# Optimization experiments

Hardware: AMD Instinct MI355X
Metric: run time of the kernel (lower is better)

## Reference

```python
import jax, jax.numpy as jnp
import numpy as np

E = 8          # num_experts
K = 2          # top_k
CAP = 0.8      # capacity_ratio
LN_EPS = 1e-6


def setup_inputs() -> dict:
    key = jax.random.key(0)
    ks = jax.random.split(key, 6)
    N, C, H, W = 64, 384, 32, 32
    Hd = 4 * C
    x = jax.random.normal(ks[0], (N, C, H, W), jnp.float32)
    conv_w = jax.random.normal(ks[1], (7, 7, 1, C), jnp.float32) * 0.05  # HWIO, depthwise
    conv_b = jnp.zeros((C,), jnp.float32)
    ln_g = jnp.ones((C,), jnp.float32)
    ln_b = jnp.zeros((C,), jnp.float32)
    gate_w = jax.random.normal(ks[2], (E, C), jnp.float32) * 0.02
    w1 = jax.random.normal(ks[3], (E, C, Hd), jnp.float32) * 0.02
    b1 = jnp.zeros((E, Hd), jnp.float32)
    w2 = jax.random.normal(ks[4], (E, Hd, C), jnp.float32) * 0.02
    b2 = jnp.zeros((E, C), jnp.float32)
    layer_scale = jnp.ones((C, 1, 1), jnp.float32) * 1e-6
    return dict(x=x, conv_w=conv_w, conv_b=conv_b, ln_g=ln_g, ln_b=ln_b,
                gate_w=gate_w, w1=w1, b1=b1, w2=w2, b2=b2, layer_scale=layer_scale)


def reference(x, conv_w, conv_b, ln_g, ln_b, gate_w, w1, b1, w2, b2, layer_scale):
    N, C, H, W = x.shape
    # depthwise 7x7 conv, pad 3
    h = jax.lax.conv_general_dilated(
        x, conv_w, window_strides=(1, 1), padding=[(3, 3), (3, 3)],
        dimension_numbers=('NCHW', 'HWIO', 'NCHW'), feature_group_count=C)
    h = h + conv_b[None, :, None, None]
    h = h.transpose(0, 2, 3, 1)  # NHWC
    # LayerNorm over channels
    mu = h.mean(-1, keepdims=True)
    var = ((h - mu) ** 2).mean(-1, keepdims=True)
    h = (h - mu) * jax.lax.rsqrt(var + LN_EPS) * ln_g + ln_b

    T = N * H * W
    x_flat = h.reshape(T, C)

    # Router (eval mode: no aux loss)
    logits = x_flat @ gate_w.T                    # [T, E]
    probs = jax.nn.softmax(logits, axis=-1)
    priority = probs.max(-1)                       # [T]
    topv, topi = jax.lax.top_k(logits, K)          # [T, K]
    weights = jax.nn.softmax(topv, axis=-1)        # [T, K]
    order = jnp.argsort(-priority)                 # descending priority

    # Dispatch: layout k-major like torch (order.repeat(K), topi[order].T.reshape(-1))
    token_idx = jnp.tile(order, K)                 # [M]
    expert_id = topi[order].T.reshape(-1)          # [M]
    gate = weights[order].T.reshape(-1)            # [M]
    M = K * T
    perm = jnp.argsort(expert_id, stable=True)
    token_idx = token_idx[perm]
    expert_id = expert_id[perm]
    gate = gate[perm]

    Be = int(round(K * T * CAP / E))               # static capacity per expert
    counts = jnp.bincount(expert_id, length=E)
    starts = jnp.cumsum(counts) - counts
    pos = jnp.arange(M) - starts[expert_id]
    keep = pos < Be
    slot = jnp.where(keep, expert_id * Be + pos, E * Be)  # dropped -> trash slot

    disp_tok = jnp.zeros((E * Be + 1,), jnp.int32).at[slot].set(token_idx.astype(jnp.int32))
    disp_gate = jnp.zeros((E * Be + 1,), x_flat.dtype).at[slot].set(gate)
    disp_tok = disp_tok[:-1].reshape(E, Be)
    disp_gate = disp_gate[:-1].reshape(E, Be)      # 0 for unfilled slots

    # Grouped expert MLP
    x_e = x_flat[disp_tok]                         # [E, Be, C]
    hid = jax.nn.gelu(jnp.einsum('ebc,ech->ebh', x_e, w1) + b1[:, None, :], approximate=False)
    y = (jnp.einsum('ebh,ehc->ebc', hid, w2) + b2[:, None, :]) * disp_gate[:, :, None]

    # Combine (scatter-add); unfilled slots contribute 0 (gate==0)
    out = jnp.zeros((T, C), x_flat.dtype).at[disp_tok.reshape(-1)].add(y.reshape(-1, C))

    out = out.reshape(N, H, W, C).transpose(0, 3, 1, 2)  # back to NCHW
    return x + layer_scale[None] * out
```

## Files before the change

### kernel.cpp

```cpp
#include <hip/hip_runtime.h>


typedef unsigned int u32;
typedef unsigned long long u64;
typedef unsigned short u16;
typedef __attribute__((ext_vector_type(8))) __bf16 bf16x8;
typedef __attribute__((ext_vector_type(4))) float f32x4;

#define T_TOK 65536
#define C_DIM 384
#define HD 1536
#define BE 13107
#define BP 13184

__device__ __forceinline__ u16 f2bf(float f) {
  u32 u = __float_as_uint(f);
  u32 r = (u + 0x7FFFu + ((u >> 16) & 1u)) >> 16;
  return (u16)r;
}
__device__ __forceinline__ float bf2f(u16 b) { return __uint_as_float(((u32)b) << 16); }

__device__ __forceinline__ u32 cvtpk(float a, float b) {
  u32 r;
  asm("v_cvt_pk_bf16_f32 %0, %1, %2" : "=v"(r) : "v"(a), "v"(b));
  return r;
}

__global__ __launch_bounds__(256) void k_conv(const float* __restrict__ x,
                                              const float* __restrict__ cw,
                                              const float* __restrict__ cb,
                                              float* __restrict__ hconv) {
  __shared__ float xp[38 * 38];
  int b = blockIdx.x;
  int c = b % 384;
  int tid = threadIdx.x;
  float w49[49];
#pragma unroll
  for (int i = 0; i < 49; i++) w49[i] = cw[i * 384 + c];
  float bias = cb[c];
  for (int i = tid; i < 38 * 38; i += 256) xp[i] = 0.0f;
  __syncthreads();
  const float* xsrc = x + (size_t)b * 1024;
  {
    float4 v = *(const float4*)&xsrc[tid * 4];
    int yy = tid >> 3, xx = (tid & 7) * 4;
    float* d = &xp[(yy + 3) * 38 + xx + 3];
    d[0] = v.x; d[1] = v.y; d[2] = v.z; d[3] = v.w;
  }
  __syncthreads();
  int cl = tid & 31, r0 = (tid >> 5) << 2;
  float o0 = bias, o1 = bias, o2 = bias, o3 = bias;
  const float* colbase = &xp[r0 * 38 + cl];
#pragma unroll
  for (int kx = 0; kx < 7; kx++) {
    float v[10];
#pragma unroll
    for (int k = 0; k < 10; k++) v[k] = colbase[k * 38 + kx];
#pragma unroll
    for (int ky = 0; ky < 7; ky++) {
      float wt = w49[ky * 7 + kx];
      o0 += wt * v[ky + 0];
      o1 += wt * v[ky + 1];
      o2 += wt * v[ky + 2];
      o3 += wt * v[ky + 3];
    }
  }
  float* dst = &hconv[(size_t)b * 1024 + r0 * 32 + cl];
  dst[0] = o0;
  dst[32] = o1;
  dst[64] = o2;
  dst[96] = o3;
}

__global__ __launch_bounds__(256) void k_ln(const float* __restrict__ hconv,
                                            const float* __restrict__ lng,
                                            const float* __restrict__ lnb,
                                            u16* __restrict__ xln) {
  __shared__ float tile[384 * 33];
  int nb = blockIdx.x;
  int n = nb >> 5, y = nb & 31;
  int tid = threadIdx.x;
  const float* src = hconv + (size_t)n * 384 * 1024 + (y << 5);
  for (int i = tid; i < 12288; i += 256) {
    int c = i >> 5, w = i & 31;
    tile[c * 33 + w] = src[(size_t)c * 1024 + w];
  }
  __syncthreads();
  int wv = tid >> 6, lane = tid & 63;
  for (int w = wv; w < 32; w += 4) {
    float v[6];
    float s = 0.f, s2 = 0.f;
#pragma unroll
    for (int k = 0; k < 6; k++) {
      float t = tile[(lane + (k << 6)) * 33 + w];
      v[k] = t; s += t; s2 += t * t;
    }
#pragma unroll
    for (int off = 32; off > 0; off >>= 1) {
      s += __shfl_xor(s, off, 64);
      s2 += __shfl_xor(s2, off, 64);
    }
    float mu = s * (1.0f / 384.0f);
    float var = s2 * (1.0f / 384.0f) - mu * mu;
    float r = rsqrtf(var + 1e-6f);
    size_t t0 = ((size_t)nb << 5) + w;
#pragma unroll
    for (int k = 0; k < 6; k++) {
      int c = lane + (k << 6);
      float o = (v[k] - mu) * r * lng[c] + lnb[c];
      xln[t0 * 384 + c] = f2bf(o);
    }
  }
}

__global__ __launch_bounds__(256) void k_router(const u16* __restrict__ xln,
                                                const float* __restrict__ gw,
                                                u32* __restrict__ keys, u32* __restrict__ vals,
                                                u32* __restrict__ topi,
                                                float* __restrict__ g1, float* __restrict__ g2) {
  __shared__ float gwl[8 * 384];
  int tid = threadIdx.x;
  for (int i = tid; i < 3072; i += 256) gwl[i] = gw[i];
  __syncthreads();
  int wv = tid >> 6, lane = tid & 63;
  int t = (blockIdx.x << 2) + wv;
  float acc[8] = {0, 0, 0, 0, 0, 0, 0, 0};
#pragma unroll
  for (int k = 0; k < 6; k++) {
    int c = lane + (k << 6);
    float xv = bf2f(xln[(size_t)t * 384 + c]);
#pragma unroll
    for (int e = 0; e < 8; e++) acc[e] += xv * gwl[e * 384 + c];
  }
#pragma unroll
  for (int off = 32; off > 0; off >>= 1) {
#pragma unroll
    for (int e = 0; e < 8; e++) acc[e] += __shfl_xor(acc[e], off, 64);
  }
  if (lane == 0) {
    float v1 = -1e30f, v2 = -1e30f;
    int e1 = 0, e2 = 0;
#pragma unroll
    for (int e = 0; e < 8; e++) {
      float l = acc[e];
      if (l > v1) { v2 = v1; e2 = e1; v1 = l; e1 = e; }
      else if (l > v2) { v2 = l; e2 = e; }
    }
    float sum = 0.f;
#pragma unroll
    for (int e = 0; e < 8; e++) sum += __expf(acc[e] - v1);
    float p = 1.0f / sum;
    float ew = __expf(v2 - v1);
    float w1 = 1.0f / (1.0f + ew);
    keys[t] = (~__float_as_uint(p)) >> 16;
    vals[t] = (u32)t;
    topi[t] = (u32)e1 | ((u32)e2 << 8);
    g1[t] = w1;
    g2[t] = ew * w1;
  }
}

__global__ __launch_bounds__(256) void k_hist(const u32* __restrict__ keys,
                                              u32* __restrict__ hist, int shift) {
  __shared__ u32 h[256];
  int tid = threadIdx.x;
  h[tid] = 0;
  __syncthreads();
  u32 key = keys[((size_t)blockIdx.x << 8) + tid];
  atomicAdd(&h[(key >> shift) & 255u], 1u);
  __syncthreads();
  hist[(size_t)tid * gridDim.x + blockIdx.x] = h[tid];
}

__global__ __launch_bounds__(256) void k_scan_rows(u32* __restrict__ data,
                                                   u32* __restrict__ totals, int nb) {
  __shared__ u32 ws[256];
  int d = blockIdx.x, tid = threadIdx.x;
  int seg = nb >> 8;
  u32 base = (u32)d * nb + tid * seg;
  u32 v[2] = {0, 0};
  u32 s = 0;
  for (int i = 0; i < seg; i++) { v[i] = data[base + i]; s += v[i]; }
  ws[tid] = s;
  __syncthreads();
  for (int dd = 1; dd < 256; dd <<= 1) {
    u32 t = (tid >= dd) ? ws[tid - dd] : 0u;
    __syncthreads();
    ws[tid] += t;
    __syncthreads();
  }
  if (tid == 255) totals[d] = ws[255];
  u32 run = (tid > 0) ? ws[tid - 1] : 0u;
  for (int i = 0; i < seg; i++) {
    u32 tmp = v[i];
    data[base + i] = run;
    run += tmp;
  }
}

__global__ __launch_bounds__(256) void k_scan_digits(const u32* __restrict__ totals,
                                                     u32* __restrict__ dbase) {
  __shared__ u32 ws[256];
  int tid = threadIdx.x;
  ws[tid] = totals[tid];
  __syncthreads();
  for (int dd = 1; dd < 256; dd <<= 1) {
    u32 t = (tid >= dd) ? ws[tid - dd] : 0u;
    __syncthreads();
    ws[tid] += t;
    __syncthreads();
  }
  dbase[tid] = (tid > 0) ? ws[tid - 1] : 0u;
}

__global__ __launch_bounds__(256) void k_scatter(const u32* __restrict__ kin,
                                                 const u32* __restrict__ vin,
                                                 u32* __restrict__ kout, u32* __restrict__ vout,
                                                 const u32* __restrict__ scanned,
                                                 const u32* __restrict__ dbase, int shift) {
  __shared__ u32 cnt[4 * 256];
  int tid = threadIdx.x;
  int w = tid >> 6, l = tid & 63;
  int g = (blockIdx.x << 8) + tid;
  u32 key = kin[g], val = vin[g];
  u32 d = (key >> shift) & 255u;
  for (int i = tid; i < 1024; i += 256) cnt[i] = 0u;
  __syncthreads();
  u64 match = ~0ull;
#pragma unroll
  for (int b = 0; b < 8; b++) {
    int bit = (d >> b) & 1;
    u64 bal = __ballot(bit);
    match &= bit ? bal : ~bal;
  }
  u32 rw = __popcll(match & ((1ull << l) - 1ull));
  if (rw == 0) cnt[(w << 8) + d] = (u32)__popcll(match);
  __syncthreads();
  u32 pre = 0;
  for (int w2 = 0; w2 < w; w2++) pre += cnt[(w2 << 8) + d];
  u32 pos = dbase[d] + scanned[(size_t)d * gridDim.x + blockIdx.x] + pre + rw;
  kout[pos] = key;
  vout[pos] = val;
}

__global__ __launch_bounds__(256) void k_entries(const u32* __restrict__ order,
                                                 const u32* __restrict__ topi,
                                                 const float* __restrict__ g1,
                                                 const float* __restrict__ g2,
                                                 u32* __restrict__ ee, u32* __restrict__ et,
                                                 float* __restrict__ eg) {
  int m = (blockIdx.x << 8) + threadIdx.x;
  int i = m & 65535, k = m >> 16;
  u32 tok = order[i];
  u32 pk = topi[tok];
  ee[m] = k ? ((pk >> 8) & 255u) : (pk & 255u);
  et[m] = tok;
  eg[m] = k ? g2[tok] : g1[tok];
}

__global__ __launch_bounds__(256) void k_dispatch(const u32* __restrict__ ee,
                                                  const u32* __restrict__ et,
                                                  const float* __restrict__ eg,
                                                  const u32* __restrict__ scanned,
                                                  int* __restrict__ dtok, float* __restrict__ dgate,
                                                  int* __restrict__ inv) {
  __shared__ u32 cnt[4 * 8];
  int tid = threadIdx.x;
  int w = tid >> 6, l = tid & 63;
  int m = (blockIdx.x << 8) + tid;
  u32 e = ee[m];
  if (tid < 32) cnt[tid] = 0u;
  __syncthreads();
  u64 match = ~0ull;
#pragma unroll
  for (int b = 0; b < 3; b++) {
    int bit = (e >> b) & 1;
    u64 bal = __ballot(bit);
    match &= bit ? bal : ~bal;
  }
  u32 rw = __popcll(match & ((1ull << l) - 1ull));
  if (rw == 0) cnt[(w << 3) + e] = (u32)__popcll(match);
  __syncthreads();
  u32 pre = 0;
  for (int w2 = 0; w2 < w; w2++) pre += cnt[(w2 << 3) + e];
  u32 pos = scanned[(size_t)e * gridDim.x + blockIdx.x] + pre + rw;
  if (pos < (u32)BE) {
    int slot = (int)e * BP + (int)pos;
    dtok[slot] = (int)et[m];
    dgate[slot] = eg[m];
    inv[et[m] * 2 + (m >> 16)] = slot;
  }
}

__global__ __launch_bounds__(256) void k_pack(const float* __restrict__ w,
                                              u16* __restrict__ wp, int NKK, int S) {
  __shared__ float tile[32 * 132];
  int e = blockIdx.y;
  int bx = blockIdx.x;
  int by = bx / NKK, kk = bx - by * NKK;
  int tid = threadIdx.x;
  const float* src = w + ((size_t)e * NKK * 32 + (size_t)kk * 32) * S + by * 128;
  for (int i = tid; i < 4096; i += 256) {
    int r = i >> 7, c = i & 127;
    tile[r * 132 + c] = src[(size_t)r * S + c];
  }
  __syncthreads();
  u16* dst = wp + ((size_t)e * gridDim.x + bx) * 4096;
#pragma unroll
  for (int h = 0; h < 2; h++) {
    int f = tid + (h << 8);
    int lane6 = f & 63, grp = f >> 6;
    int m15 = lane6 & 15, kq = lane6 >> 4;
    u16 o[8];
#pragma unroll
    for (int j = 0; j < 8; j++) o[j] = f2bf(tile[(kq * 8 + j) * 132 + grp * 16 + m15]);
    *(uint4*)&dst[f * 8] = *(const uint4*)o;
  }
}

__global__ __launch_bounds__(256) void k_gather(const u16* __restrict__ xln,
                                                const int* __restrict__ dtok,
                                                u16* __restrict__ apack, int e0) {
  __shared__ int stok[128];
  int b = blockIdx.x;
  int zloc = b / 103, bx = b - zloc * 103;
  int e = e0 + zloc;
  int tid = threadIdx.x;
  if (tid < 128) stok[tid] = dtok[e * BP + bx * 128 + tid];
  __syncthreads();
  u16* dst = apack + (size_t)b * 12 * 4096;
  int f0 = tid, f1 = tid + 256;
  int g0 = f0 >> 6, l0 = f0 & 63;
  int g1 = f1 >> 6, l1 = f1 & 63;
  int tokA = stok[g0 * 16 + (l0 & 15)];
  int tokB = stok[g1 * 16 + (l1 & 15)];
  const u16* sA = xln + (size_t)tokA * 384 + (l0 >> 4) * 8;
  const u16* sB = xln + (size_t)tokB * 384 + (l1 >> 4) * 8;
  u16* dA = dst + f0 * 8;
  u16* dB = dst + f1 * 8;
#pragma unroll
  for (int kk = 0; kk < 12; kk++) {
    *(uint4*)(dA + kk * 4096) = *(const uint4*)(sA + kk * 32);
    *(uint4*)(dB + kk * 4096) = *(const uint4*)(sB + kk * 32);
  }
}

__global__ __launch_bounds__(256) void k_gemm1(const u16* __restrict__ apack,
                                               const u16* __restrict__ w1p,
                                               const float* __restrict__ b1,
                                               u16* __restrict__ hid, int e0) {
  __shared__ u16 rpw[4 * 4608];
  int tid = threadIdx.x;
  int bid = blockIdx.x;
  int lg = (bid & 7) * 618 + (bid >> 3);
  int z = lg / 1236;
  int rr = lg - z * 1236;
  int bx = rr / 12;
  int by = rr - bx * 12;
  int e = e0 + z;
  int wv = tid >> 6, lane = tid & 63;
  int wm = wv & 1, wn = wv >> 1;
  int quad = lane >> 4, c15 = lane & 15;
  const u16* ap = apack + ((size_t)(z * 103 + bx) * 12) * 4096 + (wm * 4) * 512 + lane * 8;
  const u16* bp = w1p + ((size_t)(e * 12 + by) * 12) * 4096 + (wn * 4) * 512 + lane * 8;
  float4 bias4[4];
#pragma unroll
  for (int j = 0; j < 4; j++)
    bias4[j] = *(const float4*)&b1[e * HD + by * 128 + wn * 64 + j * 16 + quad * 4];
  f32x4 acc[4][4];
#pragma unroll
  for (int i = 0; i < 4; i++)
#pragma unroll
    for (int j = 0; j < 4; j++) acc[i][j] = (f32x4){0.f, 0.f, 0.f, 0.f};

#pragma unroll 4
  for (int kk = 0; kk < 12; kk++) {
    bf16x8 af[4], bfr[4];
#pragma unroll
    for (int i = 0; i < 4; i++) af[i] = *(const bf16x8*)(ap + kk * 4096 + i * 512);
#pragma unroll
    for (int j = 0; j < 4; j++) bfr[j] = *(const bf16x8*)(bp + kk * 4096 + j * 512);
    __builtin_amdgcn_s_setprio(1);
#pragma unroll
    for (int i = 0; i < 4; i++)
#pragma unroll
      for (int j = 0; j < 4; j++)
        acc[i][j] = __builtin_amdgcn_mfma_f32_16x16x32_bf16(bfr[j], af[i], acc[i][j], 0, 0, 0);
    __builtin_amdgcn_s_setprio(0);
  }

  u16* prp = &rpw[wv * 4608];
#pragma unroll
  for (int j = 0; j < 4; j++) {
    float4 b4 = bias4[j];
    int ncol = j * 16 + quad * 4;
#pragma unroll
    for (int i = 0; i < 4; i++) {
      int mrow = i * 16 + c15;
      float v0 = acc[i][j][0] + b4.x;
      float v1 = acc[i][j][1] + b4.y;
      float v2 = acc[i][j][2] + b4.z;
      float v3 = acc[i][j][3] + b4.w;
      v0 *= __builtin_amdgcn_rcpf(1.0f + __expf(-1.702f * v0));
      v1 *= __builtin_amdgcn_rcpf(1.0f + __expf(-1.702f * v1));
      v2 *= __builtin_amdgcn_rcpf(1.0f + __expf(-1.702f * v2));
      v3 *= __builtin_amdgcn_rcpf(1.0f + __expf(-1.702f * v3));
      uint2 pk;
      pk.x = cvtpk(v0, v1);
      pk.y = cvtpk(v2, v3);
      *(uint2*)&prp[mrow * 72 + ncol] = pk;
    }
  }
  u16* hb = hid + ((size_t)(z * 103 + bx) * 48 + by * 4 + wn * 2) * 4096 + (wm * 4) * 512 + lane * 8;
#pragma unroll
  for (int k2 = 0; k2 < 2; k2++)
#pragma unroll
    for (int gs = 0; gs < 4; gs++) {
      uint4 v = *(const uint4*)&prp[(gs * 16 + c15) * 72 + k2 * 32 + quad * 8];
      *(uint4*)(hb + (size_t)k2 * 4096 + gs * 512) = v;
    }
}

__global__ __launch_bounds__(256) void k_gemm2(const u16* __restrict__ hid,
                                               const u16* __restrict__ w2p,
                                               const float* __restrict__ b2,
                                               const float* __restrict__ dgate,
                                               u16* __restrict__ yb, int e0) {
  __shared__ u16 rpw[4 * 4608];
  int tid = threadIdx.x;
  int bid = blockIdx.x;
  int xcd = bid & 7;
  int lg = xcd * 154 + (xcd < 4 ? xcd : 4) + (bid >> 3);
  int z = lg / 309;
  int rr = lg - z * 309;
  int bx = rr / 3;
  int byn = rr - bx * 3;
  int e = e0 + z;
  int wv = tid >> 6, lane = tid & 63;
  int wm = wv & 1, wn = wv >> 1;
  int quad = lane >> 4, c15 = lane & 15;
  const u16* ap = hid + ((size_t)(z * 103 + bx) * 48) * 4096 + (wm * 4) * 512 + lane * 8;
  const u16* bp = w2p + ((size_t)(e * 3 + byn) * 48) * 4096 + (wn * 4) * 512 + lane * 8;
  float4 bias4[4];
#pragma unroll
  for (int j = 0; j < 4; j++)
    bias4[j] = *(const float4*)&b2[e * 384 + byn * 128 + wn * 64 + j * 16 + quad * 4];
  float gv[4];
#pragma unroll
  for (int i = 0; i < 4; i++) gv[i] = dgate[e * BP + bx * 128 + wm * 64 + i * 16 + c15];
  f32x4 acc[4][4];
#pragma unroll
  for (int i = 0; i < 4; i++)
#pragma unroll
    for (int j = 0; j < 4; j++) acc[i][j] = (f32x4){0.f, 0.f, 0.f, 0.f};

#pragma unroll 4
  for (int kk = 0; kk < 48; kk++) {
    bf16x8 af[4], bfr[4];
#pragma unroll
    for (int i = 0; i < 4; i++) af[i] = *(const bf16x8*)(ap + kk * 4096 + i * 512);
#pragma unroll
    for (int j = 0; j < 4; j++) bfr[j] = *(const bf16x8*)(bp + kk * 4096 + j * 512);
    __builtin_amdgcn_s_setprio(1);
#pragma unroll
    for (int i = 0; i < 4; i++)
#pragma unroll
      for (int j = 0; j < 4; j++)
        acc[i][j] = __builtin_amdgcn_mfma_f32_16x16x32_bf16(bfr[j], af[i], acc[i][j], 0, 0, 0);
    __builtin_amdgcn_s_setprio(0);
  }

  u16* prp = &rpw[wv * 4608];
#pragma unroll
  for (int j = 0; j < 4; j++) {
    float4 b4 = bias4[j];
    int ncol = j * 16 + quad * 4;
#pragma unroll
    for (int i = 0; i < 4; i++) {
      int mrow = i * 16 + c15;
      float g = gv[i];
      float v0 = (acc[i][j][0] + b4.x) * g;
      float v1 = (acc[i][j][1] + b4.y) * g;
      float v2 = (acc[i][j][2] + b4.z) * g;
      float v3 = (acc[i][j][3] + b4.w) * g;
      uint2 pk;
      pk.x = cvtpk(v0, v1);
      pk.y = cvtpk(v2, v3);
      *(uint2*)&prp[mrow * 72 + ncol] = pk;
    }
  }
  u16* ybase = yb + ((size_t)(e * BP + bx * 128 + wm * 64)) * 384 + byn * 128 + wn * 64;
#pragma unroll
  for (int it = 0; it < 8; it++) {
    int r = it * 8 + (lane >> 3);
    int n0 = (lane & 7) * 8;
    uint4 v = *(const uint4*)&prp[r * 72 + n0];
    *(uint4*)(ybase + (size_t)r * 384 + n0) = v;
  }
}

__global__ __launch_bounds__(256) void k_final(const float* __restrict__ x,
                                               const u16* __restrict__ yb,
                                               const int* __restrict__ inv,
                                               const float* __restrict__ ls,
                                               float* __restrict__ out) {
  __shared__ float tile[32 * 385];
  __shared__ int sl[64];
  int nb = blockIdx.x;
  int n = nb >> 5, yy = nb & 31;
  int tid = threadIdx.x;
  int t0 = nb << 5;
  if (tid < 64) sl[tid] = inv[t0 * 2 + tid];
  __syncthreads();
  for (int idx = tid; idx < 1536; idx += 256) {
    int w = idx / 48;
    int cc = (idx - w * 48) << 3;
    float a[8] = {0, 0, 0, 0, 0, 0, 0, 0};
#pragma unroll
    for (int k = 0; k < 2; k++) {
      int s = sl[(w << 1) + k];
      if (s >= 0) {
        uint4 v = *(const uint4*)&yb[(size_t)s * 384 + cc];
        const u16* pv = (const u16*)&v;
#pragma unroll
        for (int j = 0; j < 8; j++) a[j] += bf2f(pv[j]);
      }
    }
    float* tp = &tile[w * 385 + cc];
#pragma unroll
    for (int j = 0; j < 8; j++) tp[j] = a[j];
  }
  __syncthreads();
  for (int i2 = tid; i2 < 3072; i2 += 256) {
    int c = i2 >> 3, w4 = (i2 & 7) << 2;
    size_t o = ((((size_t)n * 384 + c) << 5) + yy) * 32 + w4;
    float4 xv = *(const float4*)&x[o];
    float lsv = ls[c];
    float4 r;
    r.x = xv.x + lsv * tile[(w4 + 0) * 385 + c];
    r.y = xv.y + lsv * tile[(w4 + 1) * 385 + c];
    r.z = xv.z + lsv * tile[(w4 + 2) * 385 + c];
    r.w = xv.w + lsv * tile[(w4 + 3) * 385 + c];
    *(float4*)&out[o] = r;
  }
}

extern "C" void kernel_launch(void* const* d_in, const int* in_sizes, int n_in,
                              void* d_out, int out_size, void* d_ws, size_t ws_size,
                              hipStream_t stream) {
  (void)in_sizes; (void)n_in; (void)out_size; (void)ws_size;
  const float* x     = (const float*)d_in[0];
  const float* convw = (const float*)d_in[1];
  const float* convb = (const float*)d_in[2];
  const float* lng   = (const float*)d_in[3];
  const float* lnb   = (const float*)d_in[4];
  const float* gw    = (const float*)d_in[5];
  const float* w1    = (const float*)d_in[6];
  const float* b1    = (const float*)d_in[7];
  const float* w2    = (const float*)d_in[8];
  const float* b2    = (const float*)d_in[9];
  const float* ls    = (const float*)d_in[10];
  float* out = (float*)d_out;

  char* p = (char*)d_ws;
  size_t o = 0;
  auto alloc = [&](size_t b) { void* r = p + o; o += (b + 255) & ~(size_t)255; return r; };
  u16* xln    = (u16*)alloc((size_t)T_TOK * C_DIM * 2);
  u16* w1p    = (u16*)alloc((size_t)8 * 144 * 4096 * 2);
  u16* w2p    = (u16*)alloc((size_t)8 * 144 * 4096 * 2);
  u16* hid    = (u16*)alloc((size_t)4 * BP * HD * 2);
  u16* yb     = (u16*)alloc((size_t)8 * BP * 384 * 2);
  u16* apack  = (u16*)alloc((size_t)4 * 103 * 12 * 4096 * 2);
  u32* keysA  = (u32*)alloc((size_t)T_TOK * 4);
  u32* keysB  = (u32*)alloc((size_t)T_TOK * 4);
  u32* valsA  = (u32*)alloc((size_t)T_TOK * 4);
  u32* valsB  = (u32*)alloc((size_t)T_TOK * 4);
  u32* topi   = (u32*)alloc((size_t)T_TOK * 4);
  float* g1   = (float*)alloc((size_t)T_TOK * 4);
  float* g2   = (float*)alloc((size_t)T_TOK * 4);
  u32* hist   = (u32*)alloc((size_t)256 * 512 * 4);
  u32* totals = (u32*)alloc((size_t)256 * 4);
  u32* dbase  = (u32*)alloc((size_t)256 * 4);
  u32* ee     = (u32*)alloc((size_t)131072 * 4);
  u32* et     = (u32*)alloc((size_t)131072 * 4);
  float* eg   = (float*)alloc((size_t)131072 * 4);
  int* dtok   = (int*)alloc((size_t)8 * BP * 4);
  float* dgate= (float*)alloc((size_t)8 * BP * 4);
  int* inv    = (int*)alloc((size_t)T_TOK * 2 * 4);

  float* hconv = (float*)hid;

  k_conv<<<24576, 256, 0, stream>>>(x, convw, convb, hconv);
  k_ln<<<2048, 256, 0, stream>>>(hconv, lng, lnb, xln);
  k_router<<<16384, 256, 0, stream>>>(xln, gw, keysA, valsA, topi, g1, g2);

  u32 *ki = keysA, *vi = valsA, *ko = keysB, *vo = valsB;
  for (int pass = 0; pass < 2; pass++) {
    int shift = pass * 8;
    k_hist<<<256, 256, 0, stream>>>(ki, hist, shift);
    k_scan_rows<<<256, 256, 0, stream>>>(hist, totals, 256);
    k_scan_digits<<<1, 256, 0, stream>>>(totals, dbase);
    k_scatter<<<256, 256, 0, stream>>>(ki, vi, ko, vo, hist, dbase, shift);
    u32* t1 = ki; ki = ko; ko = t1;
    u32* t2 = vi; vi = vo; vo = t2;
  }
  k_entries<<<512, 256, 0, stream>>>(vi, topi, g1, g2, ee, et, eg);
  k_hist<<<512, 256, 0, stream>>>(ee, hist, 0);
  k_scan_rows<<<256, 256, 0, stream>>>(hist, totals, 512);
  hipMemsetAsync(dtok, 0, (size_t)8 * BP * 4, stream);
  hipMemsetAsync(dgate, 0, (size_t)8 * BP * 4, stream);
  hipMemsetAsync(inv, 0xFF, (size_t)T_TOK * 2 * 4, stream);
  k_dispatch<<<512, 256, 0, stream>>>(ee, et, eg, hist, dtok, dgate, inv);

  k_pack<<<dim3(144, 8), 256, 0, stream>>>(w1, w1p, 12, 1536);
  k_pack<<<dim3(144, 8), 256, 0, stream>>>(w2, w2p, 48, 384);

  for (int g = 0; g < 2; g++) {
    k_gather<<<412, 256, 0, stream>>>(xln, dtok, apack, g * 4);
    k_gemm1<<<4944, 256, 0, stream>>>(apack, w1p, b1, hid, g * 4);
    k_gemm2<<<1236, 256, 0, stream>>>(hid, w2p, b2, dgate, yb, g * 4);
  }
  k_final<<<2048, 256, 0, stream>>>(x, yb, inv, ls, out);
}
```

Before: 782.6 us.

## Stage expert GEMM operands through LDS with triple-buffered async global_load_lds

Result: faster. 712.2 us (-9.0%).

```diff
diff --git a/kernel.cpp b/kernel.cpp
--- a/kernel.cpp
+++ b/kernel.cpp
@@ -24,6 +24,11 @@
   u32 r;
   asm("v_cvt_pk_bf16_f32 %0, %1, %2" : "=v"(r) : "v"(a), "v"(b));
   return r;
+}
+
+__device__ __forceinline__ void gl16(const void* g, void* l) {
+  __builtin_amdgcn_global_load_lds((const __attribute__((address_space(1))) void*)g,
+                                   (__attribute__((address_space(3))) void*)l, 16, 0, 0);
 }
 
 __global__ __launch_bounds__(256) void k_conv(const float* __restrict__ x,
@@ -349,7 +354,7 @@
                                                const u16* __restrict__ w1p,
                                                const float* __restrict__ b1,
                                                u16* __restrict__ hid, int e0) {
-  __shared__ u16 rpw[4 * 4608];
+  __shared__ __align__(16) char smem[49152];
   int tid = threadIdx.x;
   int bid = blockIdx.x;
   int lg = (bid & 7) * 618 + (bid >> 3);
@@ -361,8 +366,8 @@
   int wv = tid >> 6, lane = tid & 63;
   int wm = wv & 1, wn = wv >> 1;
   int quad = lane >> 4, c15 = lane & 15;
-  const u16* ap = apack + ((size_t)(z * 103 + bx) * 12) * 4096 + (wm * 4) * 512 + lane * 8;
-  const u16* bp = w1p + ((size_t)(e * 12 + by) * 12) * 4096 + (wn * 4) * 512 + lane * 8;
+  const u16* asrc = apack + ((size_t)(z * 103 + bx) * 12) * 4096;
+  const u16* bsrc = w1p + ((size_t)(e * 12 + by) * 12) * 4096;
   float4 bias4[4];
 #pragma unroll
   for (int j = 0; j < 4; j++)
@@ -373,13 +378,28 @@
 #pragma unroll
     for (int j = 0; j < 4; j++) acc[i][j] = (f32x4){0.f, 0.f, 0.f, 0.f};
 
-#pragma unroll 4
-  for (int kk = 0; kk < 12; kk++) {
+  char* const bb0 = smem;
+  char* const bb1 = smem + 16384;
+  char* const bb2 = smem + 32768;
+
+  auto issue = [&](int kk, char* buf) {
+    short* As = (short*)buf;
+    short* Bs = (short*)(buf + 8192);
+    const u16* a = asrc + kk * 4096;
+    const u16* b = bsrc + kk * 4096;
+    gl16(a + tid * 8, &As[tid * 8]);
+    gl16(a + (tid + 256) * 8, &As[(tid + 256) * 8]);
+    gl16(b + tid * 8, &Bs[tid * 8]);
+    gl16(b + (tid + 256) * 8, &Bs[(tid + 256) * 8]);
+  };
+  auto compute = [&](char* buf) {
+    short* As = (short*)buf;
+    short* Bs = (short*)(buf + 8192);
     bf16x8 af[4], bfr[4];
 #pragma unroll
-    for (int i = 0; i < 4; i++) af[i] = *(const bf16x8*)(ap + kk * 4096 + i * 512);
-#pragma unroll
-    for (int j = 0; j < 4; j++) bfr[j] = *(const bf16x8*)(bp + kk * 4096 + j * 512);
+    for (int i = 0; i < 4; i++) af[i] = *(const bf16x8*)&As[((((wm << 2) + i) << 6) | lane) * 8];
+#pragma unroll
+    for (int j = 0; j < 4; j++) bfr[j] = *(const bf16x8*)&Bs[((((wn << 2) + j) << 6) | lane) * 8];
     __builtin_amdgcn_s_setprio(1);
 #pragma unroll
     for (int i = 0; i < 4; i++)
@@ -387,9 +407,37 @@
       for (int j = 0; j < 4; j++)
         acc[i][j] = __builtin_amdgcn_mfma_f32_16x16x32_bf16(bfr[j], af[i], acc[i][j], 0, 0, 0);
     __builtin_amdgcn_s_setprio(0);
-  }
-
-  u16* prp = &rpw[wv * 4608];
+  };
+
+  asm volatile("s_waitcnt vmcnt(0) lgkmcnt(0)" ::: "memory");
+  __builtin_amdgcn_sched_barrier(0);
+  issue(0, bb0);
+  issue(1, bb1);
+#define STEP1(tt, ib, cb)                                \
+  issue(tt + 2, ib);                                     \
+  asm volatile("s_waitcnt vmcnt(8)" ::: "memory");       \
+  __builtin_amdgcn_sched_barrier(0);                     \
+  __builtin_amdgcn_s_barrier();                          \
+  compute(cb);                                           \
+  __builtin_amdgcn_s_barrier();
+  for (int t0 = 0; t0 < 9; t0 += 3) {
+    STEP1(t0, bb2, bb0)
+    STEP1(t0 + 1, bb0, bb1)
+    STEP1(t0 + 2, bb1, bb2)
+  }
+  STEP1(9, bb2, bb0)
+#undef STEP1
+  asm volatile("s_waitcnt vmcnt(4)" ::: "memory");
+  __builtin_amdgcn_sched_barrier(0);
+  __builtin_amdgcn_s_barrier();
+  compute(bb1);
+  asm volatile("s_waitcnt vmcnt(0)" ::: "memory");
+  __builtin_amdgcn_sched_barrier(0);
+  __builtin_amdgcn_s_barrier();
+  compute(bb2);
+  __syncthreads();
+
+  u16* prp = (u16*)smem + wv * 4608;
 #pragma unroll
   for (int j = 0; j < 4; j++) {
     float4 b4 = bias4[j];
@@ -426,7 +474,7 @@
                                                const float* __restrict__ b2,
                                                const float* __restrict__ dgate,
                                                u16* __restrict__ yb, int e0) {
-  __shared__ u16 rpw[4 * 4608];
+  __shared__ __align__(16) char smem[49152];
   int tid = threadIdx.x;
   int bid = blockIdx.x;
   int xcd = bid & 7;
@@ -439,8 +487,8 @@
   int wv = tid >> 6, lane = tid & 63;
   int wm = wv & 1, wn = wv >> 1;
   int quad = lane >> 4, c15 = lane & 15;
-  const u16* ap = hid + ((size_t)(z * 103 + bx) * 48) * 4096 + (wm * 4) * 512 + lane * 8;
-  const u16* bp = w2p + ((size_t)(e * 3 + byn) * 48) * 4096 + (wn * 4) * 512 + lane * 8;
+  const u16* asrc = hid + ((size_t)(z * 103 + bx) * 48) * 4096;
+  const u16* bsrc = w2p + ((size_t)(e * 3 + byn) * 48) * 4096;
   float4 bias4[4];
 #pragma unroll
   for (int j = 0; j < 4; j++)
@@ -454,13 +502,28 @@
 #pragma unroll
     for (int j = 0; j < 4; j++) acc[i][j] = (f32x4){0.f, 0.f, 0.f, 0.f};
 
-#pragma unroll 4
-  for (int kk = 0; kk < 48; kk++) {
+  char* const bb0 = smem;
+  char* const bb1 = smem + 16384;
+  char* const bb2 = smem + 32768;
+
+  auto issue = [&](int kk, char* buf) {
+    short* As = (short*)buf;
+    short* Bs = (short*)(buf + 8192);
+    const u16* a = asrc + kk * 4096;
+    const u16* b = bsrc + kk * 4096;
+    gl16(a + tid * 8, &As[tid * 8]);
+    gl16(a + (tid + 256) * 8, &As[(tid + 256) * 8]);
+    gl16(b + tid * 8, &Bs[tid * 8]);
+    gl16(b + (tid + 256) * 8, &Bs[(tid + 256) * 8]);
+  };
+  auto compute = [&](char* buf) {
+    short* As = (short*)buf;
+    short* Bs = (short*)(buf + 8192);
     bf16x8 af[4], bfr[4];
 #pragma unroll
-    for (int i = 0; i < 4; i++) af[i] = *(const bf16x8*)(ap + kk * 4096 + i * 512);
-#pragma unroll
-    for (int j = 0; j < 4; j++) bfr[j] = *(const bf16x8*)(bp + kk * 4096 + j * 512);
+    for (int i = 0; i < 4; i++) af[i] = *(const bf16x8*)&As[((((wm << 2) + i) << 6) | lane) * 8];
+#pragma unroll
+    for (int j = 0; j < 4; j++) bfr[j] = *(const bf16x8*)&Bs[((((wn << 2) + j) << 6) | lane) * 8];
     __builtin_amdgcn_s_setprio(1);
 #pragma unroll
     for (int i = 0; i < 4; i++)
@@ -468,9 +531,37 @@
       for (int j = 0; j < 4; j++)
         acc[i][j] = __builtin_amdgcn_mfma_f32_16x16x32_bf16(bfr[j], af[i], acc[i][j], 0, 0, 0);
     __builtin_amdgcn_s_setprio(0);
-  }
-
-  u16* prp = &rpw[wv * 4608];
+  };
+
+  asm volatile("s_waitcnt vmcnt(0) lgkmcnt(0)" ::: "memory");
+  __builtin_amdgcn_sched_barrier(0);
+  issue(0, bb0);
+  issue(1, bb1);
+#define STEP2(tt, ib, cb)                                \
+  issue(tt + 2, ib);                                     \
+  asm volatile("s_waitcnt vmcnt(8)" ::: "memory");       \
+  __builtin_amdgcn_sched_barrier(0);                     \
+  __builtin_amdgcn_s_barrier();                          \
+  compute(cb);                                           \
+  __builtin_amdgcn_s_barrier();
+  for (int t0 = 0; t0 < 45; t0 += 3) {
+    STEP2(t0, bb2, bb0)
+    STEP2(t0 + 1, bb0, bb1)
+    STEP2(t0 + 2, bb1, bb2)
+  }
+  STEP2(45, bb2, bb0)
+#undef STEP2
+  asm volatile("s_waitcnt vmcnt(4)" ::: "memory");
+  __builtin_amdgcn_sched_barrier(0);
+  __builtin_amdgcn_s_barrier();
+  compute(bb1);
+  asm volatile("s_waitcnt vmcnt(0)" ::: "memory");
+  __builtin_amdgcn_sched_barrier(0);
+  __builtin_amdgcn_s_barrier();
+  compute(bb2);
+  __syncthreads();
+
+  u16* prp = (u16*)smem + wv * 4608;
 #pragma unroll
   for (int j = 0; j < 4; j++) {
     float4 b4 = bias4[j];
```
